# Performance work log

Measured on AMD Instinct MI355X. Metric: run time of the kernel, lower is better.

The kernel has to match this reference:

```python
import jax, jax.numpy as jnp
import numpy as np
from jax import lax

B = 64            # batch size
IMG = 128         # image H=W
C_IN = 3          # channels (also conv kernel size in original code)
Q_DIM = 11
A_DIM = 10
CONV = [24, 24, 24, 24]
KS = 3
EPS = 1e-5
G_IN = (CONV[-1] + 2) * 2 + Q_DIM  # 63


def _lin_init(key, fin, fout):
    kw, kb = jax.random.split(key)
    w = jax.random.normal(kw, (fin, fout), jnp.float32) / np.sqrt(fin).astype(np.float32)
    b = jax.random.normal(kb, (fout,), jnp.float32) * 0.01
    return w, b


def _conv_init(key, cin, cout):
    kw, kb = jax.random.split(key)
    w = jax.random.normal(kw, (cout, cin, KS, KS), jnp.float32) / np.sqrt(cin * KS * KS).astype(np.float32)
    b = jax.random.normal(kb, (cout,), jnp.float32) * 0.01
    return w, b


def setup_inputs() -> dict:
    key = jax.random.key(0)
    ks = jax.random.split(key, 16)
    inp = {
        'img': jax.random.normal(ks[0], (B, C_IN, IMG, IMG), jnp.float32),
        'q': jax.random.normal(ks[1], (B, Q_DIM), jnp.float32),
    }
    cins = [C_IN] + CONV[:-1]
    for li in range(4):
        w, b = _conv_init(ks[2 + li], cins[li], CONV[li])
        inp[f'cw{li+1}'], inp[f'cb{li+1}'] = w, b
        inp[f'bg{li+1}'] = jnp.ones((CONV[li],), jnp.float32)
        inp[f'bb{li+1}'] = jnp.zeros((CONV[li],), jnp.float32)
    gins = [G_IN, 256, 256, 256]
    for li in range(4):
        w, b = _lin_init(ks[6 + li], gins[li], 256)
        inp[f'gw{li+1}'], inp[f'gb{li+1}'] = w, b
    fins, fouts = [256, 256, 256], [256, 256, A_DIM]
    for li in range(3):
        w, b = _lin_init(ks[10 + li], fins[li], fouts[li])
        inp[f'fw{li+1}'], inp[f'fb{li+1}'] = w, b
    return inp


def _conv_block(x, w, b, g, bb):
    # conv(stride=2, pad=1) -> relu -> batchnorm (train-mode batch stats)
    x = lax.conv_general_dilated(x, w, (2, 2), [(1, 1), (1, 1)],
                                 dimension_numbers=('NCHW', 'OIHW', 'NCHW'))
    x = jax.nn.relu(x + b[None, :, None, None])
    m = jnp.mean(x, axis=(0, 2, 3), keepdims=True)
    v = jnp.var(x, axis=(0, 2, 3), keepdims=True)
    return g[None, :, None, None] * (x - m) * jax.lax.rsqrt(v + EPS) + bb[None, :, None, None]


def _forward(img, q,
             cw1, cb1, bg1, bb1, cw2, cb2, bg2, bb2,
             cw3, cb3, bg3, bb3, cw4, cb4, bg4, bb4,
             gw1, gb1, gw2, gb2, gw3, gb3, gw4, gb4,
             fw1, fb1, fw2, fb2, fw3, fb3):
    x = _conv_block(img, cw1, cb1, bg1, bb1)
    x = _conv_block(x, cw2, cb2, bg2, bb2)
    x = _conv_block(x, cw3, cb3, bg3, bb3)
    x = _conv_block(x, cw4, cb4, bg4, bb4)        # [B, K, d, d]
    d = x.shape[2]
    N = d * d
    Kc = x.shape[1]
    # objects: o at flat index i corresponds to pixel (i//d, i%d) -> row-major reshape
    objs = x.reshape(B, Kc, N).transpose(0, 2, 1)           # [B, N, K]
    idx = jnp.arange(N)
    coords = jnp.stack([(idx // d).astype(jnp.float32) / d,
                        (idx % d).astype(jnp.float32) / d], axis=1)  # [N, 2]
    o = jnp.concatenate([objs, jnp.broadcast_to(coords[None], (B, N, 2))], axis=-1)  # [B, N, K+2]
    F = Kc + 2
    oi = jnp.broadcast_to(o[:, :, None, :], (B, N, N, F))
    oj = jnp.broadcast_to(o[:, None, :, :], (B, N, N, F))
    qb = jnp.broadcast_to(q[:, None, None, :], (B, N, N, Q_DIM))
    pair = jnp.concatenate([oi, oj, qb], axis=-1)           # [B, N, N, 2F+Q]
    h = jax.nn.relu(jnp.einsum('bijf,fh->bijh', pair, gw1) + gb1)
    h = jax.nn.relu(h @ gw2 + gb2)
    h = jax.nn.relu(h @ gw3 + gb3)
    h = jax.nn.relu(h @ gw4 + gb4)
    g = jnp.mean(h, axis=(1, 2))                            # mean over all N*N pairs -> [B, 256]
    # f_phi (dropout as identity / eval mode)
    g = jax.nn.relu(g @ fw1 + fb1)
    g = jax.nn.relu(g @ fw2 + fb2)
    logits = g @ fw3 + fb3
    return logits


def reference(img, q,
              cw1, cb1, bg1, bb1, cw2, cb2, bg2, bb2,
              cw3, cb3, bg3, bb3, cw4, cb4, bg4, bb4,
              gw1, gb1, gw2, gb2, gw3, gb3, gw4, gb4,
              fw1, fb1, fw2, fb2, fw3, fb3):
    return _forward(img, q,
                    cw1, cb1, bg1, bb1, cw2, cb2, bg2, bb2,
                    cw3, cb3, bg3, bb3, cw4, cb4, bg4, bb4,
                    gw1, gb1, gw2, gb2, gw3, gb3, gw4, gb4,
                    fw1, fb1, fw2, fb2, fw3, fb3)
```

## Files before the change

### kernel.cpp

```cpp
#include <hip/hip_runtime.h>
#include <hip/hip_bf16.h>

#define EPS_BN 1e-5f

typedef __bf16 bf16_t;
typedef __bf16 bf16x4 __attribute__((ext_vector_type(4)));
typedef __bf16 bf16x8 __attribute__((ext_vector_type(8)));
typedef float floatx16 __attribute__((ext_vector_type(16)));

__global__ __launch_bounds__(256) void prep_kernel(
    const float* __restrict__ q, const float* __restrict__ gw1,
    const float* __restrict__ gb1, const float* __restrict__ g2,
    const float* __restrict__ g3, const float* __restrict__ g4,
    float* __restrict__ wq, bf16_t* __restrict__ wpack)
{
    int blk = blockIdx.x, t = threadIdx.x;
    {
        float acc = gb1[t];
        #pragma unroll
        for (int d = 0; d < 11; d++)
            acc = fmaf(q[blk * 11 + d], gw1[(52 + d) * 256 + t], acc);
        wq[blk * 256 + t] = acc;
    }
    for (int idx = blk * 3072 + t; idx < blk * 3072 + 3072; idx += 256) {
        int layer = idx >> 16;
        int rem = idx & 65535;
        int col = rem & 255;
        int k = rem >> 8;
        const float* gw = (layer == 0) ? g2 : ((layer == 1) ? g3 : g4);
        float v = gw[k * 256 + col];
        int cg = col >> 5, l31 = col & 31;
        int kt = k >> 4, l2 = (k >> 3) & 1, e = k & 7;
        int lane = l2 * 32 + l31;
        wpack[(((layer * 8 + cg) * 16 + kt) * 64 + lane) * 8 + e] = (bf16_t)v;
    }
}

__global__ __launch_bounds__(256) void fin_kernel(
    const float* __restrict__ part, int P, float inv_n,
    const float* __restrict__ gamma, const float* __restrict__ beta,
    float* __restrict__ scsh)
{
    int c = blockIdx.x;
    int t = threadIdx.x;
    float s1 = 0.f, s2 = 0.f;
    for (int p = t; p < P; p += 256) {
        s1 += part[p * 48 + 2 * c];
        s2 += part[p * 48 + 2 * c + 1];
    }
    #pragma unroll
    for (int off = 32; off > 0; off >>= 1) {
        s1 += __shfl_xor(s1, off);
        s2 += __shfl_xor(s2, off);
    }
    __shared__ float r1[4], r2[4];
    int lane = t & 63, w = t >> 6;
    if (lane == 0) { r1[w] = s1; r2[w] = s2; }
    __syncthreads();
    if (t == 0) {
        float a1 = r1[0] + r1[1] + r1[2] + r1[3];
        float a2 = r2[0] + r2[1] + r2[2] + r2[3];
        float m = a1 * inv_n;
        float var = a2 * inv_n - m * m;
        float sc = gamma[c] * rsqrtf(var + EPS_BN);
        scsh[c] = sc;
        scsh[24 + c] = fmaf(-m, sc, beta[c]);
    }
}

template<int CIN, int HOUT, int OY_PER, int CO_PER, bool FOLD>
__global__ __launch_bounds__(256) void conv_kernel(
    const float* __restrict__ in, const float* __restrict__ scsh_in,
    const float* __restrict__ w, const float* __restrict__ bias,
    float* __restrict__ out, float* __restrict__ part_out)
{
    const int HIN = 2 * HOUT, ROWS = 2 * OY_PER + 3, RW = 2 * HOUT + 2;
    const int TILES = HOUT / OY_PER;
    const int WPC = (HOUT * OY_PER) / 64;
    int b = blockIdx.x / TILES, tile = blockIdx.x % TILES;
    int oy0 = tile * OY_PER;
    __shared__ float tin[CIN][ROWS][RW];
    __shared__ float scf[24], shf[24];
    __shared__ float red[4][CO_PER * 2];
    int t = threadIdx.x;
    if (FOLD) {
        if (t < 24) { scf[t] = scsh_in[t]; shf[t] = scsh_in[24 + t]; }
        __syncthreads();
    }
    const int total = CIN * ROWS * RW;
    int iyb = 2 * oy0 - 1;
    #pragma unroll 2
    for (int idx = t; idx < total; idx += 256) {
        int rx = idx % RW;
        int rem = idx / RW;
        int ry = rem % ROWS;
        int ci = rem / ROWS;
        int iy = iyb + ry, ix = rx - 1;
        float v = 0.f;
        if ((unsigned)iy < (unsigned)HIN && (unsigned)ix < (unsigned)HIN) {
            float raw = in[(b * CIN + ci) * HIN * HIN + iy * HIN + ix];
            v = FOLD ? fmaf(raw, scf[ci], shf[ci]) : raw;
        }
        tin[ci][ry][rx] = v;
    }
    __syncthreads();
    int ox = t % HOUT;
    int oyl = (t / HOUT) % OY_PER;
    int cog = t / (HOUT * OY_PER);
    const float* wp = w + cog * CO_PER * CIN * 9;
    float acc[CO_PER];
    #pragma unroll
    for (int r = 0; r < CO_PER; r++) acc[r] = bias[cog * CO_PER + r];
    for (int ci = 0; ci < CIN; ci++)
        #pragma unroll
        for (int ky = 0; ky < 3; ky++)
            #pragma unroll
            for (int kx = 0; kx < 3; kx++) {
                float v = tin[ci][2 * oyl + ky][2 * ox + kx];
                #pragma unroll
                for (int r = 0; r < CO_PER; r++)
                    acc[r] = fmaf(v, wp[(r * CIN + ci) * 9 + ky * 3 + kx], acc[r]);
            }
    int oy = oy0 + oyl;
    float s1[CO_PER], s2[CO_PER];
    #pragma unroll
    for (int r = 0; r < CO_PER; r++) {
        float v = fmaxf(acc[r], 0.f);
        out[((b * 24 + cog * CO_PER + r) * HOUT + oy) * HOUT + ox] = v;
        s1[r] = v;
        s2[r] = v * v;
    }
    int lane = t & 63, w_id = t >> 6;
    #pragma unroll
    for (int r = 0; r < CO_PER; r++) {
        float a = s1[r], c2 = s2[r];
        #pragma unroll
        for (int off = 32; off > 0; off >>= 1) {
            a += __shfl_xor(a, off);
            c2 += __shfl_xor(c2, off);
        }
        if (lane == 0) { red[w_id][r * 2] = a; red[w_id][r * 2 + 1] = c2; }
    }
    __syncthreads();
    if (t < 48) {
        int ch = t >> 1, st = t & 1;
        int cg = ch / CO_PER, r = ch % CO_PER;
        float v = 0.f;
        #pragma unroll
        for (int k = 0; k < WPC; k++) v += red[cg * WPC + k][r * 2 + st];
        part_out[blockIdx.x * 48 + t] = v;
    }
}

__global__ __launch_bounds__(256) void uv_kernel(
    const float* __restrict__ x4, const float* __restrict__ scsh4,
    const float* __restrict__ gw1, float* __restrict__ U, float* __restrict__ V)
{
    int b = blockIdx.x >> 2, n0 = (blockIdx.x & 3) * 16;
    __shared__ float o[16][26];
    int t = threadIdx.x;
    for (int idx = t; idx < 16 * 26; idx += 256) {
        int n = idx / 26, f = idx % 26;
        int ng = n0 + n;
        float val;
        if (f < 24)
            val = fmaf(x4[(b * 24 + f) * 64 + ng], scsh4[f], scsh4[24 + f]);
        else if (f == 24) val = (float)(ng >> 3) * 0.125f;
        else              val = (float)(ng & 7) * 0.125f;
        o[n][f] = val;
    }
    __syncthreads();
    float g1u[26], g1v[26];
    #pragma unroll
    for (int f = 0; f < 26; f++) {
        g1u[f] = gw1[f * 256 + t];
        g1v[f] = gw1[(26 + f) * 256 + t];
    }
    for (int n = 0; n < 16; n++) {
        float u = 0.f, v = 0.f;
        #pragma unroll
        for (int f = 0; f < 26; f++) {
            float of = o[n][f];
            u = fmaf(of, g1u[f], u);
            v = fmaf(of, g1v[f], v);
        }
        int ng = n0 + n;
        U[(b * 64 + ng) * 256 + t] = u;
        V[(b * 64 + ng) * 256 + t] = v;
    }
}

__global__ __launch_bounds__(512, 4) void pair_kernel(
    const float* __restrict__ U, const float* __restrict__ V,
    const float* __restrict__ wq, const bf16_t* __restrict__ wpack,
    const float* __restrict__ gb2, const float* __restrict__ gb3,
    const float* __restrict__ gb4, float* __restrict__ partial)
{
    __shared__ __align__(16) bf16_t hA[128][264];
    __shared__ float csum[2][256];
    int blk = blockIdx.x;
    int b = blk >> 5;
    int i0 = (blk & 31) * 2;
    int t = threadIdx.x;

    {
        int c4 = (t & 63) * 4;
        int jh = t >> 6;
        float4 wq4 = *(const float4*)(wq + b * 256 + c4);
        float4 u0 = *(const float4*)(U + (b * 64 + i0) * 256 + c4);
        float4 u1 = *(const float4*)(U + (b * 64 + i0 + 1) * 256 + c4);
        u0.x += wq4.x; u0.y += wq4.y; u0.z += wq4.z; u0.w += wq4.w;
        u1.x += wq4.x; u1.y += wq4.y; u1.z += wq4.z; u1.w += wq4.w;
        const float* Vb = V + (b * 64) * 256 + c4;
        for (int j = jh * 8; j < jh * 8 + 8; j++) {
            float4 v = *(const float4*)(Vb + j * 256);
            bf16x4 h0, h1;
            h0[0] = (bf16_t)fmaxf(u0.x + v.x, 0.f);
            h0[1] = (bf16_t)fmaxf(u0.y + v.y, 0.f);
            h0[2] = (bf16_t)fmaxf(u0.z + v.z, 0.f);
            h0[3] = (bf16_t)fmaxf(u0.w + v.w, 0.f);
            h1[0] = (bf16_t)fmaxf(u1.x + v.x, 0.f);
            h1[1] = (bf16_t)fmaxf(u1.y + v.y, 0.f);
            h1[2] = (bf16_t)fmaxf(u1.z + v.z, 0.f);
            h1[3] = (bf16_t)fmaxf(u1.w + v.w, 0.f);
            *(bf16x4*)&hA[j][c4] = h0;
            *(bf16x4*)&hA[64 + j][c4] = h1;
        }
    }
    __syncthreads();

    int lane = t & 63, wave = t >> 6;
    int l31 = lane & 31, l2 = lane >> 5;
    int wm = wave >> 2, wn = wave & 3;
    int r0 = wm * 64 + l31;
    const floatx16 zero16 = {0.f, 0.f, 0.f, 0.f, 0.f, 0.f, 0.f, 0.f,
                             0.f, 0.f, 0.f, 0.f, 0.f, 0.f, 0.f, 0.f};

    #pragma unroll 1
    for (int layer = 0; layer < 2; layer++) {
        const float* bias = (layer == 0) ? gb2 : gb3;
        const bf16_t* W0 = wpack + ((size_t)((layer * 8 + wn * 2) * 1024) + lane) * 8;
        const bf16_t* W1 = W0 + 8192;
        bf16x8 Wc[2], Wp[2];
        Wc[0] = *(const bf16x8*)W0;
        Wc[1] = *(const bf16x8*)W1;
        floatx16 acc[2][2];
        #pragma unroll
        for (int mt = 0; mt < 2; mt++)
            #pragma unroll
            for (int nt = 0; nt < 2; nt++) acc[mt][nt] = zero16;

        #pragma unroll
        for (int ks = 0; ks < 16; ks++) {
            if (ks < 15) {
                Wp[0] = *(const bf16x8*)(W0 + (ks + 1) * 512);
                Wp[1] = *(const bf16x8*)(W1 + (ks + 1) * 512);
            }
            bf16x8 h0 = *(const bf16x8*)&hA[r0][ks * 16 + l2 * 8];
            bf16x8 h1v = *(const bf16x8*)&hA[r0 + 32][ks * 16 + l2 * 8];
            #pragma unroll
            for (int nt = 0; nt < 2; nt++) {
                acc[0][nt] = __builtin_amdgcn_mfma_f32_32x32x16_bf16(Wc[nt], h0, acc[0][nt], 0, 0, 0);
                acc[1][nt] = __builtin_amdgcn_mfma_f32_32x32x16_bf16(Wc[nt], h1v, acc[1][nt], 0, 0, 0);
            }
            if (ks < 15) { Wc[0] = Wp[0]; Wc[1] = Wp[1]; }
        }

        __syncthreads();
        #pragma unroll
        for (int mt = 0; mt < 2; mt++) {
            int row = wm * 64 + mt * 32 + l31;
            #pragma unroll
            for (int nt = 0; nt < 2; nt++) {
                int fb = (wn * 2 + nt) * 32 + 4 * l2;
                #pragma unroll
                for (int g = 0; g < 4; g++) {
                    float4 bv = *(const float4*)(bias + fb + 8 * g);
                    bf16x4 w4;
                    w4[0] = (bf16_t)fmaxf(acc[mt][nt][4 * g + 0] + bv.x, 0.f);
                    w4[1] = (bf16_t)fmaxf(acc[mt][nt][4 * g + 1] + bv.y, 0.f);
                    w4[2] = (bf16_t)fmaxf(acc[mt][nt][4 * g + 2] + bv.z, 0.f);
                    w4[3] = (bf16_t)fmaxf(acc[mt][nt][4 * g + 3] + bv.w, 0.f);
                    *(bf16x4*)&hA[row][fb + 8 * g] = w4;
                }
            }
        }
        __syncthreads();
    }

    float colsum[2] = {0.f, 0.f};
    {
        float bcol[2];
        #pragma unroll
        for (int nt = 0; nt < 2; nt++)
            bcol[nt] = gb4[wn * 64 + nt * 32 + l31];

        floatx16 acc[2][2];
        #pragma unroll
        for (int mt = 0; mt < 2; mt++)
            #pragma unroll
            for (int nt = 0; nt < 2; nt++) acc[mt][nt] = zero16;

        const bf16_t* W0 = wpack + ((size_t)((16 + wn * 2) * 1024) + lane) * 8;
        const bf16_t* W1 = W0 + 8192;
        bf16x8 Bc2[2], Bn2[2];
        Bc2[0] = *(const bf16x8*)W0;
        Bc2[1] = *(const bf16x8*)W1;

        #pragma unroll
        for (int ks = 0; ks < 16; ks++) {
            if (ks < 15) {
                Bn2[0] = *(const bf16x8*)(W0 + (ks + 1) * 512);
                Bn2[1] = *(const bf16x8*)(W1 + (ks + 1) * 512);
            }
            bf16x8 a0 = *(const bf16x8*)&hA[r0][ks * 16 + l2 * 8];
            bf16x8 a1 = *(const bf16x8*)&hA[r0 + 32][ks * 16 + l2 * 8];
            #pragma unroll
            for (int nt = 0; nt < 2; nt++) {
                acc[0][nt] = __builtin_amdgcn_mfma_f32_32x32x16_bf16(a0, Bc2[nt], acc[0][nt], 0, 0, 0);
                acc[1][nt] = __builtin_amdgcn_mfma_f32_32x32x16_bf16(a1, Bc2[nt], acc[1][nt], 0, 0, 0);
            }
            if (ks < 15) { Bc2[0] = Bn2[0]; Bc2[1] = Bn2[1]; }
        }

        #pragma unroll
        for (int nt = 0; nt < 2; nt++) {
            float s = 0.f;
            #pragma unroll
            for (int mt = 0; mt < 2; mt++)
                #pragma unroll
                for (int reg = 0; reg < 16; reg++)
                    s += fmaxf(acc[mt][nt][reg] + bcol[nt], 0.0f);
            colsum[nt] += s;
        }
    }

    #pragma unroll
    for (int nt = 0; nt < 2; nt++)
        colsum[nt] += __shfl_xor(colsum[nt], 32);
    if (l2 == 0) {
        #pragma unroll
        for (int nt = 0; nt < 2; nt++)
            csum[wm][wn * 64 + nt * 32 + l31] = colsum[nt];
    }
    __syncthreads();
    if (t < 256)
        partial[blk * 256 + t] = csum[0][t] + csum[1][t];
}

__global__ __launch_bounds__(256) void fphi_kernel(
    const float* __restrict__ partial,
    const float* __restrict__ fw1, const float* __restrict__ fb1,
    const float* __restrict__ fw2, const float* __restrict__ fb2,
    const float* __restrict__ fw3, const float* __restrict__ fb3,
    float* __restrict__ out)
{
    int b = blockIdx.x, t = threadIdx.x;
    __shared__ float g[256], h1[256], h2[256];
    float s = 0.f;
    for (int k = 0; k < 32; k++) s += partial[(b * 32 + k) * 256 + t];
    g[t] = s * (1.0f / 4096.0f);
    __syncthreads();
    float a1 = fb1[t];
    for (int k = 0; k < 256; k++) a1 = fmaf(g[k], fw1[k * 256 + t], a1);
    h1[t] = fmaxf(a1, 0.0f);
    __syncthreads();
    float a2 = fb2[t];
    for (int k = 0; k < 256; k++) a2 = fmaf(h1[k], fw2[k * 256 + t], a2);
    h2[t] = fmaxf(a2, 0.0f);
    __syncthreads();
    if (t < 10) {
        float a3 = fb3[t];
        for (int k = 0; k < 256; k++) a3 = fmaf(h2[k], fw3[k * 10 + t], a3);
        out[b * 10 + t] = a3;
    }
}

extern "C" void kernel_launch(void* const* d_in, const int* in_sizes, int n_in,
                              void* d_out, int out_size, void* d_ws, size_t ws_size,
                              hipStream_t stream)
{
    (void)in_sizes; (void)n_in; (void)out_size; (void)ws_size;
    const float* img = (const float*)d_in[0];
    const float* q   = (const float*)d_in[1];
    const float* cw[4] = {(const float*)d_in[2],  (const float*)d_in[6],
                          (const float*)d_in[10], (const float*)d_in[14]};
    const float* cb[4] = {(const float*)d_in[3],  (const float*)d_in[7],
                          (const float*)d_in[11], (const float*)d_in[15]};
    const float* bg[4] = {(const float*)d_in[4],  (const float*)d_in[8],
                          (const float*)d_in[12], (const float*)d_in[16]};
    const float* bbv[4] = {(const float*)d_in[5],  (const float*)d_in[9],
                           (const float*)d_in[13], (const float*)d_in[17]};
    const float* gw1 = (const float*)d_in[18]; const float* gb1 = (const float*)d_in[19];
    const float* gw2 = (const float*)d_in[20]; const float* gb2 = (const float*)d_in[21];
    const float* gw3 = (const float*)d_in[22]; const float* gb3 = (const float*)d_in[23];
    const float* gw4 = (const float*)d_in[24]; const float* gb4 = (const float*)d_in[25];
    const float* fw1 = (const float*)d_in[26]; const float* fb1 = (const float*)d_in[27];
    const float* fw2 = (const float*)d_in[28]; const float* fb2 = (const float*)d_in[29];
    const float* fw3 = (const float*)d_in[30]; const float* fb3 = (const float*)d_in[31];

    float* ws  = (float*)d_ws;
    float* x1  = ws;
    float* x2  = x1 + 6291456;
    float* x3  = x2 + 1572864;
    float* x4  = x3 + 393216;
    float* U   = x4 + 98304;
    float* V   = U + 1048576;
    float* wqv = V + 1048576;
    float* part = wqv + 16384;
    float* p1  = part + 524288;
    float* p2  = p1 + 98304;
    float* p3  = p2 + 49152;
    float* p4  = p3 + 12288;
    float* scsh1 = p4 + 3072;
    float* scsh2 = scsh1 + 48;
    float* scsh3 = scsh2 + 48;
    float* scsh4 = scsh3 + 48;
    bf16_t* wpack = (bf16_t*)(scsh4 + 48);

    prep_kernel<<<64, 256, 0, stream>>>(q, gw1, gb1, gw2, gw3, gw4, wqv, wpack);
    conv_kernel<3, 64, 2, 12, false><<<2048, 256, 0, stream>>>(
        img, nullptr, cw[0], cb[0], x1, p1);
    fin_kernel<<<24, 256, 0, stream>>>(p1, 2048, 1.f / 262144.f, bg[0], bbv[0], scsh1);
    conv_kernel<24, 32, 2, 6, true><<<1024, 256, 0, stream>>>(
        x1, scsh1, cw[1], cb[1], x2, p2);
    fin_kernel<<<24, 256, 0, stream>>>(p2, 1024, 1.f / 65536.f, bg[1], bbv[1], scsh2);
    conv_kernel<24, 16, 4, 6, true><<<256, 256, 0, stream>>>(
        x2, scsh2, cw[2], cb[2], x3, p3);
    fin_kernel<<<24, 256, 0, stream>>>(p3, 256, 1.f / 16384.f, bg[2], bbv[2], scsh3);
    conv_kernel<24, 8, 8, 6, true><<<64, 256, 0, stream>>>(
        x3, scsh3, cw[3], cb[3], x4, p4);
    fin_kernel<<<24, 256, 0, stream>>>(p4, 64, 1.f / 4096.f, bg[3], bbv[3], scsh4);
    uv_kernel<<<256, 256, 0, stream>>>(x4, scsh4, gw1, U, V);
    pair_kernel<<<2048, 512, 0, stream>>>(U, V, wqv, wpack, gb2, gb3, gb4, part);
    fphi_kernel<<<64, 256, 0, stream>>>(part, fw1, fb1, fw2, fb2, fw3, fb3,
                                        (float*)d_out);
}
```

Measured before the change: 431.8 us.

## Halve pair kernel block size, each wave computes all 128 rows for its columns

The pair kernel now uses 4 waves of 256 threads instead of 8, and each wave covers all 128 pair rows for its 64 output columns. Each weight fragment loaded from global memory therefore feeds twice as many MFMAs. Biases are preloaded into the accumulators, and the column-sum reduction goes straight to global memory without a shared buffer. The price is more accumulator registers per wave (8 tiles of 16 floats) and fewer waves per block, which may lower occupancy and latency hiding.

```diff
diff --git a/kernel.cpp b/kernel.cpp
--- a/kernel.cpp
+++ b/kernel.cpp
@@ -190,14 +190,13 @@
     }
 }
 
-__global__ __launch_bounds__(512, 4) void pair_kernel(
+__global__ __launch_bounds__(256, 2) void pair_kernel(
     const float* __restrict__ U, const float* __restrict__ V,
     const float* __restrict__ wq, const bf16_t* __restrict__ wpack,
     const float* __restrict__ gb2, const float* __restrict__ gb3,
     const float* __restrict__ gb4, float* __restrict__ partial)
 {
     __shared__ __align__(16) bf16_t hA[128][264];
-    __shared__ float csum[2][256];
     int blk = blockIdx.x;
     int b = blk >> 5;
     int i0 = (blk & 31) * 2;
@@ -212,7 +211,7 @@
         u0.x += wq4.x; u0.y += wq4.y; u0.z += wq4.z; u0.w += wq4.w;
         u1.x += wq4.x; u1.y += wq4.y; u1.z += wq4.z; u1.w += wq4.w;
         const float* Vb = V + (b * 64) * 256 + c4;
-        for (int j = jh * 8; j < jh * 8 + 8; j++) {
+        for (int j = jh * 16; j < jh * 16 + 16; j++) {
             float4 v = *(const float4*)(Vb + j * 256);
             bf16x4 h0, h1;
             h0[0] = (bf16_t)fmaxf(u0.x + v.x, 0.f);
@@ -229,12 +228,8 @@
     }
     __syncthreads();
 
-    int lane = t & 63, wave = t >> 6;
+    int lane = t & 63, wn = t >> 6;
     int l31 = lane & 31, l2 = lane >> 5;
-    int wm = wave >> 2, wn = wave & 3;
-    int r0 = wm * 64 + l31;
-    const floatx16 zero16 = {0.f, 0.f, 0.f, 0.f, 0.f, 0.f, 0.f, 0.f,
-                             0.f, 0.f, 0.f, 0.f, 0.f, 0.f, 0.f, 0.f};
 
     #pragma unroll 1
     for (int layer = 0; layer < 2; layer++) {
@@ -244,11 +239,22 @@
         bf16x8 Wc[2], Wp[2];
         Wc[0] = *(const bf16x8*)W0;
         Wc[1] = *(const bf16x8*)W1;
-        floatx16 acc[2][2];
-        #pragma unroll
-        for (int mt = 0; mt < 2; mt++)
-            #pragma unroll
-            for (int nt = 0; nt < 2; nt++) acc[mt][nt] = zero16;
+
+        floatx16 acc[4][2];
+        #pragma unroll
+        for (int nt = 0; nt < 2; nt++) {
+            int fb = (wn * 2 + nt) * 32 + 4 * l2;
+            #pragma unroll
+            for (int g = 0; g < 4; g++) {
+                float4 bv = *(const float4*)(bias + fb + 8 * g);
+                acc[0][nt][4 * g + 0] = bv.x;
+                acc[0][nt][4 * g + 1] = bv.y;
+                acc[0][nt][4 * g + 2] = bv.z;
+                acc[0][nt][4 * g + 3] = bv.w;
+            }
+            #pragma unroll
+            for (int mt = 1; mt < 4; mt++) acc[mt][nt] = acc[0][nt];
+        }
 
         #pragma unroll
         for (int ks = 0; ks < 16; ks++) {
@@ -256,31 +262,32 @@
                 Wp[0] = *(const bf16x8*)(W0 + (ks + 1) * 512);
                 Wp[1] = *(const bf16x8*)(W1 + (ks + 1) * 512);
             }
-            bf16x8 h0 = *(const bf16x8*)&hA[r0][ks * 16 + l2 * 8];
-            bf16x8 h1v = *(const bf16x8*)&hA[r0 + 32][ks * 16 + l2 * 8];
-            #pragma unroll
-            for (int nt = 0; nt < 2; nt++) {
-                acc[0][nt] = __builtin_amdgcn_mfma_f32_32x32x16_bf16(Wc[nt], h0, acc[0][nt], 0, 0, 0);
-                acc[1][nt] = __builtin_amdgcn_mfma_f32_32x32x16_bf16(Wc[nt], h1v, acc[1][nt], 0, 0, 0);
-            }
+            bf16x8 h[4];
+            #pragma unroll
+            for (int mt = 0; mt < 4; mt++)
+                h[mt] = *(const bf16x8*)&hA[mt * 32 + l31][ks * 16 + l2 * 8];
+            #pragma unroll
+            for (int mt = 0; mt < 4; mt++)
+                #pragma unroll
+                for (int nt = 0; nt < 2; nt++)
+                    acc[mt][nt] = __builtin_amdgcn_mfma_f32_32x32x16_bf16(Wc[nt], h[mt], acc[mt][nt], 0, 0, 0);
             if (ks < 15) { Wc[0] = Wp[0]; Wc[1] = Wp[1]; }
         }
 
         __syncthreads();
         #pragma unroll
-        for (int mt = 0; mt < 2; mt++) {
-            int row = wm * 64 + mt * 32 + l31;
+        for (int mt = 0; mt < 4; mt++) {
+            int row = mt * 32 + l31;
             #pragma unroll
             for (int nt = 0; nt < 2; nt++) {
                 int fb = (wn * 2 + nt) * 32 + 4 * l2;
                 #pragma unroll
                 for (int g = 0; g < 4; g++) {
-                    float4 bv = *(const float4*)(bias + fb + 8 * g);
                     bf16x4 w4;
-                    w4[0] = (bf16_t)fmaxf(acc[mt][nt][4 * g + 0] + bv.x, 0.f);
-                    w4[1] = (bf16_t)fmaxf(acc[mt][nt][4 * g + 1] + bv.y, 0.f);
-                    w4[2] = (bf16_t)fmaxf(acc[mt][nt][4 * g + 2] + bv.z, 0.f);
-                    w4[3] = (bf16_t)fmaxf(acc[mt][nt][4 * g + 3] + bv.w, 0.f);
+                    w4[0] = (bf16_t)fmaxf(acc[mt][nt][4 * g + 0], 0.f);
+                    w4[1] = (bf16_t)fmaxf(acc[mt][nt][4 * g + 1], 0.f);
+                    w4[2] = (bf16_t)fmaxf(acc[mt][nt][4 * g + 2], 0.f);
+                    w4[3] = (bf16_t)fmaxf(acc[mt][nt][4 * g + 3], 0.f);
                     *(bf16x4*)&hA[row][fb + 8 * g] = w4;
                 }
             }
@@ -288,64 +295,55 @@
         __syncthreads();
     }
 
-    float colsum[2] = {0.f, 0.f};
     {
-        float bcol[2];
-        #pragma unroll
-        for (int nt = 0; nt < 2; nt++)
-            bcol[nt] = gb4[wn * 64 + nt * 32 + l31];
-
-        floatx16 acc[2][2];
-        #pragma unroll
-        for (int mt = 0; mt < 2; mt++)
-            #pragma unroll
-            for (int nt = 0; nt < 2; nt++) acc[mt][nt] = zero16;
+        floatx16 acc[4][2];
+        #pragma unroll
+        for (int nt = 0; nt < 2; nt++) {
+            float bc = gb4[wn * 64 + nt * 32 + l31];
+            #pragma unroll
+            for (int mt = 0; mt < 4; mt++)
+                #pragma unroll
+                for (int reg = 0; reg < 16; reg++)
+                    acc[mt][nt][reg] = bc;
+        }
 
         const bf16_t* W0 = wpack + ((size_t)((16 + wn * 2) * 1024) + lane) * 8;
         const bf16_t* W1 = W0 + 8192;
-        bf16x8 Bc2[2], Bn2[2];
-        Bc2[0] = *(const bf16x8*)W0;
-        Bc2[1] = *(const bf16x8*)W1;
+        bf16x8 Bc[2], Bn[2];
+        Bc[0] = *(const bf16x8*)W0;
+        Bc[1] = *(const bf16x8*)W1;
 
         #pragma unroll
         for (int ks = 0; ks < 16; ks++) {
             if (ks < 15) {
-                Bn2[0] = *(const bf16x8*)(W0 + (ks + 1) * 512);
-                Bn2[1] = *(const bf16x8*)(W1 + (ks + 1) * 512);
+                Bn[0] = *(const bf16x8*)(W0 + (ks + 1) * 512);
+                Bn[1] = *(const bf16x8*)(W1 + (ks + 1) * 512);
             }
-            bf16x8 a0 = *(const bf16x8*)&hA[r0][ks * 16 + l2 * 8];
-            bf16x8 a1 = *(const bf16x8*)&hA[r0 + 32][ks * 16 + l2 * 8];
-            #pragma unroll
-            for (int nt = 0; nt < 2; nt++) {
-                acc[0][nt] = __builtin_amdgcn_mfma_f32_32x32x16_bf16(a0, Bc2[nt], acc[0][nt], 0, 0, 0);
-                acc[1][nt] = __builtin_amdgcn_mfma_f32_32x32x16_bf16(a1, Bc2[nt], acc[1][nt], 0, 0, 0);
-            }
-            if (ks < 15) { Bc2[0] = Bn2[0]; Bc2[1] = Bn2[1]; }
+            bf16x8 a[4];
+            #pragma unroll
+            for (int mt = 0; mt < 4; mt++)
+                a[mt] = *(const bf16x8*)&hA[mt * 32 + l31][ks * 16 + l2 * 8];
+            #pragma unroll
+            for (int mt = 0; mt < 4; mt++)
+                #pragma unroll
+                for (int nt = 0; nt < 2; nt++)
+                    acc[mt][nt] = __builtin_amdgcn_mfma_f32_32x32x16_bf16(a[mt], Bc[nt], acc[mt][nt], 0, 0, 0);
+            if (ks < 15) { Bc[0] = Bn[0]; Bc[1] = Bn[1]; }
         }
 
         #pragma unroll
         for (int nt = 0; nt < 2; nt++) {
             float s = 0.f;
             #pragma unroll
-            for (int mt = 0; mt < 2; mt++)
+            for (int mt = 0; mt < 4; mt++)
                 #pragma unroll
                 for (int reg = 0; reg < 16; reg++)
-                    s += fmaxf(acc[mt][nt][reg] + bcol[nt], 0.0f);
-            colsum[nt] += s;
-        }
-    }
-
-    #pragma unroll
-    for (int nt = 0; nt < 2; nt++)
-        colsum[nt] += __shfl_xor(colsum[nt], 32);
-    if (l2 == 0) {
-        #pragma unroll
-        for (int nt = 0; nt < 2; nt++)
-            csum[wm][wn * 64 + nt * 32 + l31] = colsum[nt];
-    }
-    __syncthreads();
-    if (t < 256)
-        partial[blk * 256 + t] = csum[0][t] + csum[1][t];
+                    s += fmaxf(acc[mt][nt][reg], 0.0f);
+            s += __shfl_xor(s, 32);
+            if (l2 == 0)
+                partial[blk * 256 + wn * 64 + nt * 32 + l31] = s;
+        }
+    }
 }
 
 __global__ __launch_bounds__(256) void fphi_kernel(
@@ -432,7 +430,7 @@
         x3, scsh3, cw[3], cb[3], x4, p4);
     fin_kernel<<<24, 256, 0, stream>>>(p4, 64, 1.f / 4096.f, bg[3], bbv[3], scsh4);
     uv_kernel<<<256, 256, 0, stream>>>(x4, scsh4, gw1, U, V);
-    pair_kernel<<<2048, 512, 0, stream>>>(U, V, wqv, wpack, gb2, gb3, gb4, part);
+    pair_kernel<<<2048, 256, 0, stream>>>(U, V, wqv, wpack, gb2, gb3, gb4, part);
     fphi_kernel<<<64, 256, 0, stream>>>(part, fw1, fb1, fw2, fb2, fw3, fb3,
                                         (float*)d_out);
 }
```

New measurement: 417.3 us. -3.4%, faster.
